# Kernel optimization log

Measured on AMD Instinct MI355X. Metric: run time of the kernel, lower is better.

The kernel has to match this reference:

```python
import jax, jax.numpy as jnp
import numpy as np

B, H, W, C = 64, 14, 14, 768
HID = 4 * C            # ConvNeXt MLP hidden
E, K, R = 8, 2, 16     # num_experts, top_k, lora rank
SCALING = 16.0 / 16.0  # alpha / r


def setup_inputs() -> dict:
    key = jax.random.key(0)
    ks = jax.random.split(key, 9)
    N = B * H * W
    x = jax.random.normal(ks[0], (B, H, W, C), jnp.float32)
    p = jax.random.uniform(ks[1], (N, K), jnp.float32)
    topk_probs = p / (p.sum(-1, keepdims=True) + 1e-6)
    topk_idx = jax.random.randint(ks[2], (N, K), 0, E)
    w1 = jax.random.normal(ks[3], (C, HID), jnp.float32) * (C ** -0.5)
    b1 = jnp.zeros((HID,), jnp.float32)
    w2 = jax.random.normal(ks[4], (HID, C), jnp.float32) * (HID ** -0.5)
    b2 = jnp.zeros((C,), jnp.float32)
    w_down = jax.random.normal(ks[5], (E, C, R), jnp.float32) * (C ** -0.5)
    # torch init is zeros; use small randn so the op is numerically non-trivial
    w_up = jax.random.normal(ks[6], (E, R, C), jnp.float32) * 0.02
    return {"x": x, "topk_probs": topk_probs, "topk_idx": topk_idx,
            "w1": w1, "b1": b1, "w2": w2, "b2": b2,
            "w_down": w_down, "w_up": w_up}


def reference(x, topk_probs, topk_idx, w1, b1, w2, b2, w_down, w_up):
    # orig ConvNeXt MLP: Linear -> GELU(exact) -> Linear, pointwise over [B,H,W,C]
    h = jax.nn.gelu(jnp.einsum('bhwc,cf->bhwf', x, w1) + b1, approximate=False)
    orig = jnp.einsum('bhwf,fc->bhwc', h, w2) + b2

    N = x.shape[0] * x.shape[1] * x.shape[2]
    xf = x.reshape(N, C)  # [N, C] tokens
    # per-token combine weight for each expert: sum_k p[n,k] * 1[idx[n,k]==e]
    wt = (jax.nn.one_hot(topk_idx, E, dtype=xf.dtype) * topk_probs[..., None]).sum(1)  # [N, E]
    # dense-over-experts LoRA (vectorized form of the per-expert gather/scatter loop)
    down = jax.nn.gelu(jnp.einsum('nc,ecr->ner', xf, w_down), approximate=False)  # [N, E, R]
    up = jnp.einsum('ner,erc->nec', down, w_up) * SCALING                          # [N, E, C]
    moe = jnp.einsum('nec,ne->nc', up, wt)                                         # [N, C]
    return orig + moe.reshape(x.shape)
```

## Files before the change

### kernel.cpp

```cpp
#include <hip/hip_runtime.h>
#include <hip/hip_bf16.h>
#include <math.h>


#define NTOK   12544
#define CDIM   768
#define HIDDIM 3072
#define KBIG   3200

typedef __attribute__((ext_vector_type(8))) short bf16x8;
typedef __attribute__((ext_vector_type(4))) float f32x4;

#define GLOBAL_AS(p) ((const __attribute__((address_space(1))) void*)(p))
#define LDS_AS(p)    ((__attribute__((address_space(3))) void*)(p))
#define GLD(src, dst) __builtin_amdgcn_global_load_lds(GLOBAL_AS(src), LDS_AS(dst), 16, 0, 0)

__device__ inline unsigned short f2bf(float f) {
    unsigned int x = __float_as_uint(f);
    x += 0x7fffu + ((x >> 16) & 1u);
    return (unsigned short)(x >> 16);
}

__device__ inline float gelu_fast(float x) {
    float x3 = x * x * x;
    float u2 = 1.5957691216057308f * x + 0.07135481627260025f * x3;
    float e = __expf(-u2);
    return x * __builtin_amdgcn_rcpf(1.0f + e);
}

__global__ void __launch_bounds__(256) prep_kernel(
        const float* __restrict__ x, const float* __restrict__ w1,
        const float* __restrict__ w2, const float* __restrict__ wup,
        const float* __restrict__ wdn,
        unsigned short* __restrict__ xb, unsigned short* __restrict__ w1t,
        unsigned short* __restrict__ B2t, unsigned short* __restrict__ wdt) {
    __shared__ float tile[64][65];
    const int b = blockIdx.x, tid = threadIdx.x;
    if (b < 9408) {
        int i = b * 256 + tid;
        float4 v = ((const float4*)x)[i];
        ushort4 o;
        o.x = f2bf(v.x); o.y = f2bf(v.y); o.z = f2bf(v.z); o.w = f2bf(v.w);
        ((ushort4*)xb)[i] = o;
        return;
    }
    if (b < 10584) {
        const float* in; unsigned short* outp; int Ccols, out_ld, out_off, bx, by;
        if (b < 9984)       { int t = b - 9408;  in = w1;  outp = w1t; Ccols = 3072; out_ld = 768;  out_off = 0;    bx = t % 48; by = t / 48; }
        else if (b < 10560) { int t = b - 9984;  in = w2;  outp = B2t; Ccols = 768;  out_ld = 3200; out_off = 0;    bx = t % 12; by = t / 12; }
        else                { int t = b - 10560; in = wup; outp = B2t; Ccols = 768;  out_ld = 3200; out_off = 3072; bx = t % 12; by = t / 12; }
        const int c0 = bx * 64, r0 = by * 64;
        #pragma unroll
        for (int p = 0; p < 4; ++p) {
            int idx = p * 256 + tid;
            int r = idx >> 4, c4 = (idx & 15) * 4;
            float4 v = *(const float4*)&in[(size_t)(r0 + r) * Ccols + c0 + c4];
            tile[r][c4 + 0] = v.x; tile[r][c4 + 1] = v.y;
            tile[r][c4 + 2] = v.z; tile[r][c4 + 3] = v.w;
        }
        __syncthreads();
        #pragma unroll
        for (int p = 0; p < 2; ++p) {
            int u = p * 256 + tid;
            int cc = u >> 3, r8 = (u & 7) * 8;
            uint4 pk;
            pk.x = (unsigned)f2bf(tile[r8 + 0][cc]) | ((unsigned)f2bf(tile[r8 + 1][cc]) << 16);
            pk.y = (unsigned)f2bf(tile[r8 + 2][cc]) | ((unsigned)f2bf(tile[r8 + 3][cc]) << 16);
            pk.z = (unsigned)f2bf(tile[r8 + 4][cc]) | ((unsigned)f2bf(tile[r8 + 5][cc]) << 16);
            pk.w = (unsigned)f2bf(tile[r8 + 6][cc]) | ((unsigned)f2bf(tile[r8 + 7][cc]) << 16);
            *(uint4*)&outp[(size_t)(c0 + cc) * out_ld + out_off + r0 + r8] = pk;
        }
        return;
    }
    {
        int idx = (b - 10584) * 256 + tid;
        int j = idx / 768, c = idx - j * 768;
        int e = j >> 4, r = j & 15;
        wdt[idx] = f2bf(wdn[((size_t)e * 768 + c) * 16 + r]);
    }
}

template <int EPI, int TM>
__global__ void __launch_bounds__(TM * 2)
gemm_bt_kernel(const unsigned short* __restrict__ A, int lda,
               const unsigned short* __restrict__ Bt, int ldb,
               int kIters,
               const float* __restrict__ bias,
               unsigned short* __restrict__ apOut,
               float* __restrict__ fOut,
               const int* __restrict__ tki,
               const float* __restrict__ tkp) {
    constexpr int NT    = TM * 2;
    constexpr int ABUF  = TM * 32;
    constexpr int BBUF  = 128 * 32;
    __shared__ __align__(16) unsigned short As[2 * ABUF];
    __shared__ __align__(16) unsigned short Bs[2 * BBUF];

    const int bx = blockIdx.x, by = blockIdx.y;
    const int tid  = threadIdx.x;
    const int wave = tid >> 6;
    const int lane = tid & 63;
    const int m0 = by * TM;
    const int n0 = bx * 128;
    const int wm = (wave >> 1) * 64;
    const int wn = (wave & 1) * 64;
    const int row16 = lane & 15;
    const int quad  = lane >> 4;
    const int kch   = quad * 8;

    f32x4 acc[4][4] = {};

    const int r_s = tid >> 2;
    const int c_s = (tid & 3) * 8;
    const size_t aRow0 = (size_t)(m0 + r_s) * lda + c_s;
    const size_t aRow1 = aRow0 + (size_t)(NT / 4) * lda;
    const size_t bRow0 = (size_t)(n0 + r_s) * ldb + c_s;
    const size_t bRow1 = bRow0 + (size_t)64 * ldb;
    unsigned short* asB0 = &As[(wave * 64) * 8];
    unsigned short* asB1 = &As[(NT + wave * 64) * 8];
    unsigned short* bsB0 = &Bs[(wave * 64) * 8];
    unsigned short* bsB1 = &Bs[(256 + wave * 64) * 8];

    {
        GLD(A + aRow0, asB0);
        GLD(A + aRow1, asB1);
        GLD(Bt + bRow0, bsB0);
        if (TM == 128) GLD(Bt + bRow1, bsB1);
    }

    for (int kt = 0; kt < kIters; ++kt) {
        __syncthreads();

        if (kt + 1 < kIters) {
            const int k1 = (kt + 1) * 32;
            const int pa = ((kt + 1) & 1) * ABUF;
            const int pb = ((kt + 1) & 1) * BBUF;
            GLD(A + aRow0 + k1, asB0 + pa);
            GLD(A + aRow1 + k1, asB1 + pa);
            GLD(Bt + bRow0 + k1, bsB0 + pb);
            if (TM == 128) GLD(Bt + bRow1 + k1, bsB1 + pb);
        }

        const int ca = (kt & 1) * ABUF;
        const int cb = (kt & 1) * BBUF;
        bf16x8 af[4], bfr[4];
        #pragma unroll
        for (int mi = 0; mi < 4; ++mi)
            af[mi] = *(const bf16x8*)&As[ca + (wm + mi * 16 + row16) * 32 + kch];
        #pragma unroll
        for (int ni = 0; ni < 4; ++ni)
            bfr[ni] = *(const bf16x8*)&Bs[cb + (wn + ni * 16 + row16) * 32 + kch];

        #pragma unroll
        for (int mi = 0; mi < 4; ++mi)
            #pragma unroll
            for (int ni = 0; ni < 4; ++ni)
                acc[mi][ni] = __builtin_amdgcn_mfma_f32_16x16x32_bf16(
                    af[mi], bfr[ni], acc[mi][ni], 0, 0, 0);
    }

    #pragma unroll
    for (int mi = 0; mi < 4; ++mi) {
        #pragma unroll
        for (int i = 0; i < 4; ++i) {
            const int m = m0 + wm + mi * 16 + quad * 4 + i;
            int i0 = 0, i1 = 0; float p0 = 0.f, p1 = 0.f;
            if (EPI == 1) {
                i0 = tki[m * 2]; i1 = tki[m * 2 + 1];
                p0 = tkp[m * 2]; p1 = tkp[m * 2 + 1];
            }
            #pragma unroll
            for (int ni = 0; ni < 4; ++ni) {
                const int ncol = n0 + wn + ni * 16 + row16;
                float v = acc[mi][ni][i];
                if (EPI == 0) {
                    v = gelu_fast(v + bias[ncol]);
                    apOut[(size_t)m * KBIG + ncol] = f2bf(v);
                } else if (EPI == 1) {
                    const int e = ncol >> 4;
                    float wt = (i0 == e ? p0 : 0.f) + (i1 == e ? p1 : 0.f);
                    v = gelu_fast(v) * wt;
                    apOut[(size_t)m * KBIG + 3072 + ncol] = f2bf(v);
                } else {
                    fOut[(size_t)m * CDIM + ncol] = v + bias[ncol];
                }
            }
        }
    }
}


template <int NFRAG, int Q, bool TAILV, class Issue>
__device__ __forceinline__ void phase8(
        const char* ldsAbuf, const char* ldsBbuf, int aFB, int bFB, int swz,
        f32x4 (&acc)[8][NFRAG], bf16x8 (&bfr)[NFRAG][2], Issue issue) {
    bf16x8 af[2][2];
    #pragma unroll
    for (int f = 0; f < 2; ++f)
        #pragma unroll
        for (int k = 0; k < 2; ++k)
            af[f][k] = *(const bf16x8*)(ldsAbuf + ((aFB + Q * 4096 + f * 2048 + k * 64) ^ swz));
    if (Q == 0) {
        #pragma unroll
        for (int nf = 0; nf < NFRAG; ++nf)
            #pragma unroll
            for (int k = 0; k < 2; ++k)
                bfr[nf][k] = *(const bf16x8*)(ldsBbuf + ((bFB + nf * 2048 + k * 64) ^ swz));
    }
    issue();
    __builtin_amdgcn_s_barrier();
    asm volatile("s_waitcnt lgkmcnt(0)" ::: "memory");
    __builtin_amdgcn_sched_barrier(0);
    __builtin_amdgcn_s_setprio(1);
    #pragma unroll
    for (int f = 0; f < 2; ++f)
        #pragma unroll
        for (int nf = 0; nf < NFRAG; ++nf)
            #pragma unroll
            for (int k = 0; k < 2; ++k)
                acc[2 * Q + f][nf] = __builtin_amdgcn_mfma_f32_16x16x32_bf16(
                    af[f][k], bfr[nf][k], acc[2 * Q + f][nf], 0, 0, 0);
    __builtin_amdgcn_s_setprio(0);
    if (TAILV) {
        if constexpr (NFRAG == 4) asm volatile("s_waitcnt vmcnt(4)" ::: "memory");
        else                      asm volatile("s_waitcnt vmcnt(3)" ::: "memory");
    }
    __builtin_amdgcn_s_barrier();
    __builtin_amdgcn_sched_barrier(0);
}

template <int EPI, int NFRAG, int NBX>
__global__ void __launch_bounds__(512, 2)
gemm8_kernel(const unsigned short* __restrict__ A, int lda,
             const unsigned short* __restrict__ Bt, int ldb,
             int kTiles, const float* __restrict__ bias,
             unsigned short* __restrict__ apOut, float* __restrict__ fOut) {
    constexpr int BBYTES = NFRAG * 8192;
    __shared__ __align__(1024) char ldsraw[65536 + 2 * BBYTES];
    char* ldsA = ldsraw;
    char* ldsB = ldsraw + 65536;

    const int nwg  = gridDim.x;
    const int q    = nwg >> 3, r = nwg & 7;
    const int orig = blockIdx.x;
    const int xcd  = orig & 7, within = orig >> 3;
    const int wgid = (xcd < r ? xcd * (q + 1) : r * (q + 1) + (xcd - r) * q) + within;
    const int bx = wgid % NBX, by = wgid / NBX;

    const int tid  = threadIdx.x;
    const int wave = tid >> 6;
    const int lane = tid & 63;
    const int m0 = by * 256;
    const int n0 = bx * (NFRAG * 64);
    const int row16 = lane & 15;
    const int quad  = lane >> 4;
    const int wm = (wave >> 2) << 7;
    const int wn = (wave & 3) * (NFRAG * 16);
    const int swz = (row16 & 7) << 4;
    const int aFB = ((wm + row16) << 7) + (quad << 4);
    const int bFB = ((wn + row16) << 7) + (quad << 4);

    const int d  = tid << 4;
    const int s  = d ^ (((d >> 7) & 7) << 4);
    const int sr = s >> 7;
    const int sc = (s & 127) >> 1;
    const char* aSrc = (const char*)(A + (size_t)(m0 + sr) * lda + sc);
    const char* bSrc = (const char*)(Bt + (size_t)(n0 + sr) * ldb + sc);
    const size_t aStep = (size_t)64 * lda * 2;
    const size_t bStep = (size_t)64 * ldb * 2;
    const int ldsW = wave << 10;

    auto issueA = [&](int b, int h, int tk) {
        const char* sp = aSrc + (size_t)(2 * h) * aStep + (size_t)tk * 128;
        char* dp = ldsA + b * 32768 + h * 16384 + ldsW;
        GLD(sp, dp);
        GLD(sp + aStep, dp + 8192);
    };
    auto issueB = [&](int b, int c, int tk) {
        const char* sp = bSrc + (size_t)c * bStep + (size_t)tk * 128;
        char* dp = ldsB + b * BBYTES + c * 8192 + ldsW;
        GLD(sp, dp);
    };

    f32x4 acc[8][NFRAG] = {};

    #pragma unroll
    for (int c = 0; c < NFRAG; ++c) issueB(0, c, 0);
    issueA(0, 0, 0); issueA(0, 1, 0);
    #pragma unroll
    for (int c = 0; c < NFRAG; ++c) issueB(1, c, 1);
    if constexpr (NFRAG == 4) asm volatile("s_waitcnt vmcnt(4)" ::: "memory");
    else                      asm volatile("s_waitcnt vmcnt(3)" ::: "memory");
    __builtin_amdgcn_s_barrier();
    __builtin_amdgcn_sched_barrier(0);

    const char* A0 = ldsA;         const char* B0 = ldsB;
    const char* A1 = ldsA + 32768; const char* B1 = ldsB + BBYTES;
    const int nIter = kTiles >> 1;
    for (int it = 0; it < nIter; ++it) {
        const int t  = it * 2;
        const int t2 = (t + 2 < kTiles) ? t + 2 : 0;
        const int t3 = (t + 3 < kTiles) ? t + 3 : 0;
        bf16x8 bfr[NFRAG][2];
        phase8<NFRAG, 0, false>(A0, B0, aFB, bFB, swz, acc, bfr, [&]{ issueA(1, 0, t + 1); });
        phase8<NFRAG, 1, false>(A0, B0, aFB, bFB, swz, acc, bfr, [&]{ issueA(1, 1, t + 1); });
        phase8<NFRAG, 2, false>(A0, B0, aFB, bFB, swz, acc, bfr, [&]{ issueB(0, 0, t2); issueB(0, 1, t2); });
        phase8<NFRAG, 3, true >(A0, B0, aFB, bFB, swz, acc, bfr, [&]{
            #pragma unroll
            for (int c = 2; c < NFRAG; ++c) issueB(0, c, t2); });
        phase8<NFRAG, 0, false>(A1, B1, aFB, bFB, swz, acc, bfr, [&]{ issueA(0, 0, t2); });
        phase8<NFRAG, 1, false>(A1, B1, aFB, bFB, swz, acc, bfr, [&]{ issueA(0, 1, t2); });
        phase8<NFRAG, 2, false>(A1, B1, aFB, bFB, swz, acc, bfr, [&]{ issueB(1, 0, t3); issueB(1, 1, t3); });
        phase8<NFRAG, 3, true >(A1, B1, aFB, bFB, swz, acc, bfr, [&]{
            #pragma unroll
            for (int c = 2; c < NFRAG; ++c) issueB(1, c, t3); });
    }
    asm volatile("s_waitcnt vmcnt(0)" ::: "memory");

    float bv[NFRAG];
    #pragma unroll
    for (int nf = 0; nf < NFRAG; ++nf) bv[nf] = bias[n0 + wn + nf * 16 + row16];
    #pragma unroll
    for (int mi = 0; mi < 8; ++mi) {
        #pragma unroll
        for (int i = 0; i < 4; ++i) {
            const int m = m0 + wm + mi * 16 + quad * 4 + i;
            #pragma unroll
            for (int nf = 0; nf < NFRAG; ++nf) {
                const int col = n0 + wn + nf * 16 + row16;
                float v = acc[mi][nf][i] + bv[nf];
                if (EPI == 0) apOut[(size_t)m * KBIG + col] = f2bf(gelu_fast(v));
                else          fOut[(size_t)m * CDIM + col] = v;
            }
        }
    }
}


extern "C" void kernel_launch(void* const* d_in, const int* in_sizes, int n_in,
                              void* d_out, int out_size, void* d_ws, size_t ws_size,
                              hipStream_t stream) {
    const float* x   = (const float*)d_in[0];
    const float* tkp = (const float*)d_in[1];
    const int*   tki = (const int*)d_in[2];
    const float* w1  = (const float*)d_in[3];
    const float* b1  = (const float*)d_in[4];
    const float* w2  = (const float*)d_in[5];
    const float* b2  = (const float*)d_in[6];
    const float* wdn = (const float*)d_in[7];
    const float* wup = (const float*)d_in[8];
    float* out = (float*)d_out;

    unsigned short* xb  = (unsigned short*)d_ws;
    unsigned short* w1t = xb  + (size_t)NTOK * CDIM;
    unsigned short* B2t = w1t + (size_t)HIDDIM * CDIM;
    unsigned short* wdt = B2t + (size_t)CDIM * KBIG;
    unsigned short* Ap  = wdt + (size_t)128 * CDIM;

    prep_kernel<<<dim3(10968), 256, 0, stream>>>(x, w1, w2, wup, wdn,
                                                 xb, w1t, B2t, wdt);

    gemm_bt_kernel<1, 128><<<dim3(1, NTOK / 128), 256, 0, stream>>>(
        xb, CDIM, wdt, CDIM, CDIM / 32, nullptr, Ap, nullptr, tki, tkp);
    gemm8_kernel<0, 4, HIDDIM / 256><<<dim3((HIDDIM / 256) * (NTOK / 256)), 512, 0, stream>>>(
        xb, CDIM, w1t, CDIM, CDIM / 64, b1, Ap, nullptr);
    gemm8_kernel<2, 3, CDIM / 192><<<dim3((CDIM / 192) * (NTOK / 256)), 512, 0, stream>>>(
        Ap, KBIG, B2t, KBIG, KBIG / 64, b2, nullptr, out);
}
```

Before: 271.7 us.

## Shrink GEMM tiles to 128x192 with four-phase pipeline for higher occupancy

Replaces the 256-row, 8-phase GEMM kernel with a 128x192 tile variant that runs four phases per pair of k-tiles and uses 80 KB of LDS. Launch bounds now request 4 workgroups per CU, and the swizzled LDS offsets are precomputed once outside the loop. Both the first and second MLP GEMMs use the new kernel, which gives more workgroups and better wave-level latency hiding. In exchange, each tile reuses operands less, so more global/L2 traffic is needed per FLOP, and the tighter register budget at 4 blocks per CU could cause spills.

```diff
diff --git a/kernel.cpp b/kernel.cpp
--- a/kernel.cpp
+++ b/kernel.cpp
@@ -190,22 +190,22 @@
 }
 
 
-template <int NFRAG, int Q, bool TAILV, class Issue>
-__device__ __forceinline__ void phase8(
-        const char* ldsAbuf, const char* ldsBbuf, int aFB, int bFB, int swz,
-        f32x4 (&acc)[8][NFRAG], bf16x8 (&bfr)[NFRAG][2], Issue issue) {
+template <int P, bool TAILV, class Issue>
+__device__ __forceinline__ void phase4(
+        const char* lds, int aO0, int aO1, int bO0, int bO1,
+        f32x4 (&acc)[4][3], bf16x8 (&bfr)[3][2], Issue issue) {
     bf16x8 af[2][2];
     #pragma unroll
-    for (int f = 0; f < 2; ++f)
-        #pragma unroll
-        for (int k = 0; k < 2; ++k)
-            af[f][k] = *(const bf16x8*)(ldsAbuf + ((aFB + Q * 4096 + f * 2048 + k * 64) ^ swz));
-    if (Q == 0) {
-        #pragma unroll
-        for (int nf = 0; nf < NFRAG; ++nf)
-            #pragma unroll
-            for (int k = 0; k < 2; ++k)
-                bfr[nf][k] = *(const bf16x8*)(ldsBbuf + ((bFB + nf * 2048 + k * 64) ^ swz));
+    for (int f = 0; f < 2; ++f) {
+        af[f][0] = *(const bf16x8*)(lds + aO0 + (2 * P + f) * 2048);
+        af[f][1] = *(const bf16x8*)(lds + aO1 + (2 * P + f) * 2048);
+    }
+    if (P == 0) {
+        #pragma unroll
+        for (int nf = 0; nf < 3; ++nf) {
+            bfr[nf][0] = *(const bf16x8*)(lds + bO0 + nf * 2048);
+            bfr[nf][1] = *(const bf16x8*)(lds + bO1 + nf * 2048);
+        }
     }
     issue();
     __builtin_amdgcn_s_barrier();
@@ -215,30 +215,26 @@
     #pragma unroll
     for (int f = 0; f < 2; ++f)
         #pragma unroll
-        for (int nf = 0; nf < NFRAG; ++nf)
+        for (int nf = 0; nf < 3; ++nf)
             #pragma unroll
             for (int k = 0; k < 2; ++k)
-                acc[2 * Q + f][nf] = __builtin_amdgcn_mfma_f32_16x16x32_bf16(
-                    af[f][k], bfr[nf][k], acc[2 * Q + f][nf], 0, 0, 0);
+                acc[2 * P + f][nf] = __builtin_amdgcn_mfma_f32_16x16x32_bf16(
+                    af[f][k], bfr[nf][k], acc[2 * P + f][nf], 0, 0, 0);
     __builtin_amdgcn_s_setprio(0);
-    if (TAILV) {
-        if constexpr (NFRAG == 4) asm volatile("s_waitcnt vmcnt(4)" ::: "memory");
-        else                      asm volatile("s_waitcnt vmcnt(3)" ::: "memory");
-    }
+    if (TAILV) asm volatile("s_waitcnt vmcnt(3)" ::: "memory");
     __builtin_amdgcn_s_barrier();
     __builtin_amdgcn_sched_barrier(0);
 }
 
-template <int EPI, int NFRAG, int NBX>
-__global__ void __launch_bounds__(512, 2)
-gemm8_kernel(const unsigned short* __restrict__ A, int lda,
+template <int EPI, int NBX>
+__global__ void __launch_bounds__(512, 4)
+gemm4_kernel(const unsigned short* __restrict__ A, int lda,
              const unsigned short* __restrict__ Bt, int ldb,
              int kTiles, const float* __restrict__ bias,
              unsigned short* __restrict__ apOut, float* __restrict__ fOut) {
-    constexpr int BBYTES = NFRAG * 8192;
-    __shared__ __align__(1024) char ldsraw[65536 + 2 * BBYTES];
+    __shared__ __align__(1024) char ldsraw[81920];
     char* ldsA = ldsraw;
-    char* ldsB = ldsraw + 65536;
+    char* ldsB = ldsraw + 32768;
 
     const int nwg  = gridDim.x;
     const int q    = nwg >> 3, r = nwg & 7;
@@ -250,15 +246,17 @@
     const int tid  = threadIdx.x;
     const int wave = tid >> 6;
     const int lane = tid & 63;
-    const int m0 = by * 256;
-    const int n0 = bx * (NFRAG * 64);
+    const int m0 = by * 128;
+    const int n0 = bx * 192;
     const int row16 = lane & 15;
     const int quad  = lane >> 4;
-    const int wm = (wave >> 2) << 7;
-    const int wn = (wave & 3) * (NFRAG * 16);
+    const int wm = (wave >> 2) << 6;
+    const int wn = (wave & 3) * 48;
     const int swz = (row16 & 7) << 4;
     const int aFB = ((wm + row16) << 7) + (quad << 4);
     const int bFB = ((wn + row16) << 7) + (quad << 4);
+    const int aX0 = (aFB ^ swz),        aX1 = ((aFB + 64) ^ swz);
+    const int bX0 = (bFB ^ swz) + 32768, bX1 = ((bFB + 64) ^ swz) + 32768;
 
     const int d  = tid << 4;
     const int s  = d ^ (((d >> 7) & 7) << 4);
@@ -270,63 +268,56 @@
     const size_t bStep = (size_t)64 * ldb * 2;
     const int ldsW = wave << 10;
 
-    auto issueA = [&](int b, int h, int tk) {
-        const char* sp = aSrc + (size_t)(2 * h) * aStep + (size_t)tk * 128;
-        char* dp = ldsA + b * 32768 + h * 16384 + ldsW;
+    auto issueA = [&](int b, int tk) {
+        const char* sp = aSrc + (size_t)tk * 128;
+        char* dp = ldsA + b * 16384 + ldsW;
         GLD(sp, dp);
         GLD(sp + aStep, dp + 8192);
     };
-    auto issueB = [&](int b, int c, int tk) {
-        const char* sp = bSrc + (size_t)c * bStep + (size_t)tk * 128;
-        char* dp = ldsB + b * BBYTES + c * 8192 + ldsW;
+    auto issueB = [&](int b, int tk) {
+        const char* sp = bSrc + (size_t)tk * 128;
+        char* dp = ldsB + b * 24576 + ldsW;
         GLD(sp, dp);
+        GLD(sp + bStep, dp + 8192);
+        GLD(sp + 2 * bStep, dp + 16384);
     };
 
-    f32x4 acc[8][NFRAG] = {};
-
-    #pragma unroll
-    for (int c = 0; c < NFRAG; ++c) issueB(0, c, 0);
-    issueA(0, 0, 0); issueA(0, 1, 0);
-    #pragma unroll
-    for (int c = 0; c < NFRAG; ++c) issueB(1, c, 1);
-    if constexpr (NFRAG == 4) asm volatile("s_waitcnt vmcnt(4)" ::: "memory");
-    else                      asm volatile("s_waitcnt vmcnt(3)" ::: "memory");
+    f32x4 acc[4][3] = {};
+
+    issueB(0, 0);
+    issueA(0, 0);
+    issueB(1, 1);
+    asm volatile("s_waitcnt vmcnt(3)" ::: "memory");
     __builtin_amdgcn_s_barrier();
     __builtin_amdgcn_sched_barrier(0);
 
-    const char* A0 = ldsA;         const char* B0 = ldsB;
-    const char* A1 = ldsA + 32768; const char* B1 = ldsB + BBYTES;
     const int nIter = kTiles >> 1;
     for (int it = 0; it < nIter; ++it) {
         const int t  = it * 2;
         const int t2 = (t + 2 < kTiles) ? t + 2 : 0;
         const int t3 = (t + 3 < kTiles) ? t + 3 : 0;
-        bf16x8 bfr[NFRAG][2];
-        phase8<NFRAG, 0, false>(A0, B0, aFB, bFB, swz, acc, bfr, [&]{ issueA(1, 0, t + 1); });
-        phase8<NFRAG, 1, false>(A0, B0, aFB, bFB, swz, acc, bfr, [&]{ issueA(1, 1, t + 1); });
-        phase8<NFRAG, 2, false>(A0, B0, aFB, bFB, swz, acc, bfr, [&]{ issueB(0, 0, t2); issueB(0, 1, t2); });
-        phase8<NFRAG, 3, true >(A0, B0, aFB, bFB, swz, acc, bfr, [&]{
-            #pragma unroll
-            for (int c = 2; c < NFRAG; ++c) issueB(0, c, t2); });
-        phase8<NFRAG, 0, false>(A1, B1, aFB, bFB, swz, acc, bfr, [&]{ issueA(0, 0, t2); });
-        phase8<NFRAG, 1, false>(A1, B1, aFB, bFB, swz, acc, bfr, [&]{ issueA(0, 1, t2); });
-        phase8<NFRAG, 2, false>(A1, B1, aFB, bFB, swz, acc, bfr, [&]{ issueB(1, 0, t3); issueB(1, 1, t3); });
-        phase8<NFRAG, 3, true >(A1, B1, aFB, bFB, swz, acc, bfr, [&]{
-            #pragma unroll
-            for (int c = 2; c < NFRAG; ++c) issueB(1, c, t3); });
+        bf16x8 bfr[3][2];
+        phase4<0, false>(ldsraw, aX0, aX1, bX0, bX1, acc, bfr,
+                         [&]{ issueA(1, t + 1); });
+        phase4<1, true >(ldsraw, aX0, aX1, bX0, bX1, acc, bfr,
+                         [&]{ issueB(0, t2); });
+        phase4<0, false>(ldsraw, aX0 + 16384, aX1 + 16384, bX0 + 24576, bX1 + 24576, acc, bfr,
+                         [&]{ issueA(0, t2); });
+        phase4<1, true >(ldsraw, aX0 + 16384, aX1 + 16384, bX0 + 24576, bX1 + 24576, acc, bfr,
+                         [&]{ issueB(1, t3); });
     }
     asm volatile("s_waitcnt vmcnt(0)" ::: "memory");
 
-    float bv[NFRAG];
-    #pragma unroll
-    for (int nf = 0; nf < NFRAG; ++nf) bv[nf] = bias[n0 + wn + nf * 16 + row16];
-    #pragma unroll
-    for (int mi = 0; mi < 8; ++mi) {
+    float bv[3];
+    #pragma unroll
+    for (int nf = 0; nf < 3; ++nf) bv[nf] = bias[n0 + wn + nf * 16 + row16];
+    #pragma unroll
+    for (int mi = 0; mi < 4; ++mi) {
         #pragma unroll
         for (int i = 0; i < 4; ++i) {
             const int m = m0 + wm + mi * 16 + quad * 4 + i;
             #pragma unroll
-            for (int nf = 0; nf < NFRAG; ++nf) {
+            for (int nf = 0; nf < 3; ++nf) {
                 const int col = n0 + wn + nf * 16 + row16;
                 float v = acc[mi][nf][i] + bv[nf];
                 if (EPI == 0) apOut[(size_t)m * KBIG + col] = f2bf(gelu_fast(v));
@@ -362,8 +353,8 @@
 
     gemm_bt_kernel<1, 128><<<dim3(1, NTOK / 128), 256, 0, stream>>>(
         xb, CDIM, wdt, CDIM, CDIM / 32, nullptr, Ap, nullptr, tki, tkp);
-    gemm8_kernel<0, 4, HIDDIM / 256><<<dim3((HIDDIM / 256) * (NTOK / 256)), 512, 0, stream>>>(
+    gemm4_kernel<0, HIDDIM / 192><<<dim3((HIDDIM / 192) * (NTOK / 128)), 512, 0, stream>>>(
         xb, CDIM, w1t, CDIM, CDIM / 64, b1, Ap, nullptr);
-    gemm8_kernel<2, 3, CDIM / 192><<<dim3((CDIM / 192) * (NTOK / 256)), 512, 0, stream>>>(
+    gemm4_kernel<2, CDIM / 192><<<dim3((CDIM / 192) * (NTOK / 128)), 512, 0, stream>>>(
         Ap, KBIG, B2t, KBIG, KBIG / 64, b2, nullptr, out);
 }
```

Measured after the change: 264.2 us. 1.03x faster.
